# Optimization experiments

Measured on AMD Instinct MI355X. Metric: run time of the kernel, lower is better.

The kernel has to match this reference:

```python
import jax, jax.numpy as jnp
import numpy as np

RADIUS = 5.0
CORRECT_THRESHOLD = 0.5
NUM_CLASSES = 4
COORD_RANGE = 64.0  # keep coords in a small field so some preds actually match


def setup_inputs() -> dict:
    key = jax.random.key(0)
    k1, k2, k3, k4 = jax.random.split(key, 4)
    B, P, T = 16, 4096, 1024
    pred_cls = jax.random.randint(k1, (B, P, 1), 0, NUM_CLASSES).astype(jnp.float32)
    pred_xy = jax.random.uniform(k2, (B, P, 2), dtype=jnp.float32) * COORD_RANGE
    gt_cls = jax.random.randint(k3, (B, T, 1), 0, NUM_CLASSES).astype(jnp.float32)
    gt_xy = jax.random.uniform(k4, (B, T, 2), dtype=jnp.float32) * COORD_RANGE
    pred = jnp.concatenate([pred_cls, pred_xy], axis=-1)  # [B,P,3]
    gt = jnp.concatenate([gt_cls, gt_xy], axis=-1)        # [B,T,3]
    return {"pred": pred, "gt": gt}


def _radial_score(centers, targets):
    # centers: [B,P,2], targets: [B,T,2] -> [B,P,T]; sigmoid(1 - dist/radius)
    d = centers[:, :, None, :] - targets[:, None, :, :]
    dist = jnp.sqrt(jnp.sum(d * d, axis=-1))
    return jax.nn.sigmoid(1.0 - dist / RADIUS)


def reference(pred, gt):
    B, P, _ = pred.shape
    T = gt.shape[1]
    classes = pred[:, :, 0]          # [B,P]
    centers = pred[:, :, 1:3]        # [B,P,2]
    tclasses = gt[:, :, 0]           # [B,T]
    tcenters = gt[:, :, 1:3]         # [B,T,2]

    scores = _radial_score(centers, tcenters)                       # [B,P,T]
    valid = (scores >= CORRECT_THRESHOLD) & (
        classes[:, :, None] == tclasses[:, None, :])                # [B,P,T]

    # Greedy dedup (sort-by-score + unique on target col) keeps, per target,
    # its highest-scoring valid pred; the second unique (pred col) only drops
    # duplicate preds and never changes the set of matched pred indices.
    masked = jnp.where(valid, scores, -jnp.inf)
    best_pred = jnp.argmax(masked, axis=1)                          # [B,T]
    has_match = jnp.any(valid, axis=1)                              # [B,T]

    flat_idx = (best_pred + jnp.arange(B, dtype=best_pred.dtype)[:, None] * P).ravel()
    hits = jnp.zeros((B * P,), jnp.float32).at[flat_idx].add(
        has_match.ravel().astype(jnp.float32))
    correct = hits.reshape(B, P) > 0                                # [B,P]

    tp = correct.sum().astype(jnp.float32)
    fp = jnp.float32(B * P) - tp
    fn = jnp.float32(B * T) - tp

    eps = jnp.float32(1e-6)
    precision = (tp + eps) / (tp + eps + fp + eps)
    recall = (tp + eps) / (tp + fn + eps)
    f1 = 2.0 * precision * recall / (precision + recall)
    return 1.0 - f1
```

## Files before the change

kernel.cpp:

```cpp
#include <hip/hip_runtime.h>
#include <math.h>

#define BB 16
#define PP 4096
#define TT 1024
#define JT 16
#define QTR 1024
#define LIMKEY 0x41C80FFFu

__global__ __launch_bounds__(256) void match_kernel(const float* __restrict__ pred,
                                                    const float* __restrict__ gt,
                                                    unsigned* __restrict__ part) {
    const int blk   = blockIdx.x;
    const int b     = blk >> 6;
    const int ttile = (blk >> 2) & 15;
    const int qtr   = blk & 3;
    const int wave  = threadIdx.x >> 6;
    const int lane  = threadIdx.x & 63;
    const int tbase = ttile * 64 + wave * JT;
    const int pbase = qtr * QTR;

    const float* gb = gt + ((size_t)(b * TT + tbase)) * 3;
    float gx[JT], gy[JT];
    unsigned key[JT];
    #pragma unroll
    for (int j = 0; j < JT; ++j) {
        const float c = gb[j * 3 + 0];
        gx[j] = fmaf(c, 128.0f, gb[j * 3 + 1]);
        gy[j] = gb[j * 3 + 2];
        key[j] = 0xFFFFFFFFu;
    }

    const float* pl = pred + (size_t)b * PP * 3 + (size_t)(pbase + lane) * 3;

    #pragma unroll 4
    for (int i = 0; i < QTR / 64; ++i) {
        const float pc = pl[0];
        const float px = pl[1];
        const float py = pl[2];
        pl += 192;
        const float pxp = fmaf(pc, 128.0f, px);
        const unsigned po = (unsigned)(pbase + (i << 6) + lane);
        #pragma unroll
        for (int j = 0; j < JT; ++j) {
            const float dx = pxp - gx[j];
            const float dy = py - gy[j];
            const float d2 = fmaf(dx, dx, dy * dy);
            const unsigned kk = (__float_as_uint(d2) & 0xFFFFF000u) | po;
            key[j] = min(key[j], kk);
        }
    }

    for (int off = 32; off; off >>= 1) {
        #pragma unroll
        for (int j = 0; j < JT; ++j) {
            const unsigned o = __shfl_down(key[j], off, 64);
            key[j] = min(key[j], o);
        }
    }

    if (lane == 0) {
        #pragma unroll
        for (int j = 0; j < JT; ++j)
            part[(size_t)qtr * (BB * TT) + b * TT + tbase + j] = key[j];
    }
}

__global__ __launch_bounds__(256) void count_kernel(const unsigned* __restrict__ part,
                                                    int* __restrict__ psum) {
    __shared__ unsigned bm[PP / 32];
    if (threadIdx.x < 128) bm[threadIdx.x] = 0;
    __syncthreads();

    const int b = blockIdx.x;
    const unsigned* pb = part + b * TT;
    for (int i = threadIdx.x; i < TT; i += 256) {
        unsigned k = min(min(pb[i], pb[BB * TT + i]),
                         min(pb[2 * BB * TT + i], pb[3 * BB * TT + i]));
        if (k <= LIMKEY) {
            const unsigned p = k & 0xFFFu;
            atomicOr(&bm[p >> 5], 1u << (p & 31));
        }
    }
    __syncthreads();

    int sum = (threadIdx.x < 128) ? (int)__popc(bm[threadIdx.x]) : 0;
    for (int off = 32; off; off >>= 1) sum += __shfl_down(sum, off, 64);
    __shared__ int ss[4];
    if ((threadIdx.x & 63) == 0) ss[threadIdx.x >> 6] = sum;
    __syncthreads();
    if (threadIdx.x == 0) psum[b] = ss[0] + ss[1] + ss[2] + ss[3];
}

__global__ void f1_kernel(const int* __restrict__ psum, float* __restrict__ out) {
    int v = (threadIdx.x < BB) ? psum[threadIdx.x] : 0;
    for (int off = 32; off; off >>= 1) v += __shfl_down(v, off, 64);
    if (threadIdx.x == 0) {
        const float tp = (float)v;
        const float eps = 1e-6f;
        const float fp = (float)(BB * PP) - tp;
        const float fn = (float)(BB * TT) - tp;
        const float precision = (tp + eps) / (tp + eps + fp + eps);
        const float recall    = (tp + eps) / (tp + fn + eps);
        const float f1 = 2.0f * precision * recall / (precision + recall);
        out[0] = 1.0f - f1;
    }
}

extern "C" void kernel_launch(void* const* d_in, const int* in_sizes, int n_in,
                              void* d_out, int out_size, void* d_ws, size_t ws_size,
                              hipStream_t stream) {
    const float* pred = (const float*)d_in[0];
    const float* gt   = (const float*)d_in[1];
    float* out = (float*)d_out;

    unsigned* part = (unsigned*)d_ws;
    int* psum = (int*)((char*)d_ws + 4 * BB * TT * 4);

    match_kernel<<<BB * 16 * 4, 256, 0, stream>>>(pred, gt, part);
    count_kernel<<<BB, 256, 0, stream>>>(part, psum);
    f1_kernel<<<1, 64, 0, stream>>>(psum, out);
}
```

Baseline: 70.75 us.

## Fuse match, count and F1 kernels via last-block ticket reduction

Merges the three launches into one kernel. Each block increments an atomic ticket after writing its partial keys, and the last block to finish builds a shared-memory bitmap of matched preds for all batches, then computes the F1 loss. This removes two kernel launches and their gaps at the cost of a memset, a threadfence per block, and a serial tail where one block processes all 16K targets with an 8KB bitmap.

```diff
diff --git a/kernel.cpp b/kernel.cpp
--- a/kernel.cpp
+++ b/kernel.cpp
@@ -6,11 +6,14 @@
 #define TT 1024
 #define JT 16
 #define QTR 1024
+#define NBLK (BB * 16 * 4)
 #define LIMKEY 0x41C80FFFu
 
-__global__ __launch_bounds__(256) void match_kernel(const float* __restrict__ pred,
+__global__ __launch_bounds__(256) void fused_kernel(const float* __restrict__ pred,
                                                     const float* __restrict__ gt,
-                                                    unsigned* __restrict__ part) {
+                                                    unsigned* __restrict__ part,
+                                                    unsigned* __restrict__ ticket,
+                                                    float* __restrict__ out) {
     const int blk   = blockIdx.x;
     const int b     = blk >> 6;
     const int ttile = (blk >> 2) & 15;
@@ -64,39 +67,38 @@
         for (int j = 0; j < JT; ++j)
             part[(size_t)qtr * (BB * TT) + b * TT + tbase + j] = key[j];
     }
-}
 
-__global__ __launch_bounds__(256) void count_kernel(const unsigned* __restrict__ part,
-                                                    int* __restrict__ psum) {
-    __shared__ unsigned bm[PP / 32];
-    if (threadIdx.x < 128) bm[threadIdx.x] = 0;
+    __shared__ int is_last;
+    __threadfence();
+    if (threadIdx.x == 0)
+        is_last = (atomicAdd(ticket, 1u) == NBLK - 1);
+    __syncthreads();
+    if (!is_last) return;
+    __threadfence();
+
+    __shared__ unsigned bm[BB * PP / 32];
+    for (int i = threadIdx.x; i < BB * PP / 32; i += 256) bm[i] = 0;
     __syncthreads();
 
-    const int b = blockIdx.x;
-    const unsigned* pb = part + b * TT;
-    for (int i = threadIdx.x; i < TT; i += 256) {
-        unsigned k = min(min(pb[i], pb[BB * TT + i]),
-                         min(pb[2 * BB * TT + i], pb[3 * BB * TT + i]));
+    for (int i = threadIdx.x; i < BB * TT; i += 256) {
+        const unsigned k = min(min(part[i],              part[BB * TT + i]),
+                               min(part[2 * BB * TT + i], part[3 * BB * TT + i]));
         if (k <= LIMKEY) {
-            const unsigned p = k & 0xFFFu;
-            atomicOr(&bm[p >> 5], 1u << (p & 31));
+            const unsigned g = (unsigned)(i >> 10) * PP + (k & 0xFFFu);
+            atomicOr(&bm[g >> 5], 1u << (g & 31));
         }
     }
     __syncthreads();
 
-    int sum = (threadIdx.x < 128) ? (int)__popc(bm[threadIdx.x]) : 0;
+    int sum = 0;
+    for (int i = threadIdx.x; i < BB * PP / 32; i += 256) sum += __popc(bm[i]);
     for (int off = 32; off; off >>= 1) sum += __shfl_down(sum, off, 64);
+
     __shared__ int ss[4];
-    if ((threadIdx.x & 63) == 0) ss[threadIdx.x >> 6] = sum;
+    if (lane == 0) ss[wave] = sum;
     __syncthreads();
-    if (threadIdx.x == 0) psum[b] = ss[0] + ss[1] + ss[2] + ss[3];
-}
-
-__global__ void f1_kernel(const int* __restrict__ psum, float* __restrict__ out) {
-    int v = (threadIdx.x < BB) ? psum[threadIdx.x] : 0;
-    for (int off = 32; off; off >>= 1) v += __shfl_down(v, off, 64);
     if (threadIdx.x == 0) {
-        const float tp = (float)v;
+        const float tp = (float)(ss[0] + ss[1] + ss[2] + ss[3]);
         const float eps = 1e-6f;
         const float fp = (float)(BB * PP) - tp;
         const float fn = (float)(BB * TT) - tp;
@@ -114,10 +116,9 @@
     const float* gt   = (const float*)d_in[1];
     float* out = (float*)d_out;
 
-    unsigned* part = (unsigned*)d_ws;
-    int* psum = (int*)((char*)d_ws + 4 * BB * TT * 4);
+    unsigned* part   = (unsigned*)d_ws;
+    unsigned* ticket = (unsigned*)((char*)d_ws + 4 * BB * TT * 4);
 
-    match_kernel<<<BB * 16 * 4, 256, 0, stream>>>(pred, gt, part);
-    count_kernel<<<BB, 256, 0, stream>>>(part, psum);
-    f1_kernel<<<1, 64, 0, stream>>>(psum, out);
+    hipMemsetAsync(ticket, 0, 4, stream);
+    fused_kernel<<<NBLK, 256, 0, stream>>>(pred, gt, part, ticket, out);
 }
```

After: 151.3 us. +113.8%, slower.
